# Performance work log

Hardware: AMD Instinct MI355X
Metric: run time of the kernel (lower is better)

The kernel has to match this reference:

```python
import jax, jax.numpy as jnp
import numpy as np

N = 50000
E = 800000
TEXT_VOCAB = 7000
ACTION_DIM = 64
MAX_POS = 5120
POS_DIM = 128   # edge encoder out_dim
NODE_DIM = 128  # text_out 64 + type_out 64
EDGE_DIM = 128
H1 = 256
OUT = 32
NEG_SLOPE = 0.2


def _pos_table():
    # sinusoidal table, [MAX_POS+1, POS_DIM]; even cols = cos, odd cols = sin
    positions = np.arange(0, MAX_POS + 1, dtype=np.float32)
    inv_freq = 1.0 / (10000.0 ** (np.arange(0.0, POS_DIM, 2.0, dtype=np.float32) / POS_DIM))
    si = np.outer(positions, inv_freq)
    tab = np.zeros((MAX_POS + 1, POS_DIM), dtype=np.float32)
    tab[:, 1::2] = np.sin(si)
    tab[:, 0::2] = np.cos(si)
    return jnp.asarray(tab)


def setup_inputs() -> dict:
    key = jax.random.key(0)
    ks = jax.random.split(key, 32)
    ri = jax.random.randint
    nrm = lambda k, s, scale=0.05: (jax.random.normal(k, s, dtype=jnp.float32) * scale)
    x = jnp.stack([ri(ks[0], (N,), 0, TEXT_VOCAB + 1, dtype=jnp.int32),
                   ri(ks[1], (N,), 0, 3, dtype=jnp.int32)], axis=-1)
    edge_index = ri(ks[2], (2, E), 0, N, dtype=jnp.int32)
    edge_attr = jnp.stack([ri(ks[3], (E,), 0, 3, dtype=jnp.int32),
                           ri(ks[4], (E,), 0, MAX_POS + 1, dtype=jnp.int32)], axis=-1)
    d = {
        "x": x, "edge_index": edge_index, "edge_attr": edge_attr,
        "text_emb": nrm(ks[5], (TEXT_VOCAB + 1, 64), 1.0),
        "type_emb": nrm(ks[6], (3, 64), 1.0),
        "flow_emb": nrm(ks[7], (3, EDGE_DIM), 1.0),
        "pos_table": _pos_table(),
        "pos_W": nrm(ks[8], (POS_DIM, POS_DIM)), "pos_b": nrm(ks[9], (POS_DIM,)),
        "c1_Wl": nrm(ks[10], (NODE_DIM, H1)), "c1_bl": nrm(ks[11], (H1,)),
        "c1_Wr": nrm(ks[12], (NODE_DIM, H1)), "c1_br": nrm(ks[13], (H1,)),
        "c1_We": nrm(ks[14], (EDGE_DIM, H1)), "c1_att": nrm(ks[15], (H1,)),
        "c1_bias": nrm(ks[16], (H1,)),
        "c2_Wl": nrm(ks[17], (H1, OUT)), "c2_bl": nrm(ks[18], (OUT,)),
        "c2_Wr": nrm(ks[19], (H1, OUT)), "c2_br": nrm(ks[20], (OUT,)),
        "c2_We": nrm(ks[21], (EDGE_DIM, OUT)), "c2_att": nrm(ks[22], (OUT,)),
        "c2_bias": nrm(ks[23], (OUT,)),
        "policy_W": nrm(ks[24], (OUT, ACTION_DIM), 0.2), "policy_b": nrm(ks[25], (ACTION_DIM,)),
    }
    return d


def gatv2(h, src, dst, ea, Wl, bl, Wr, br, We, att, bias, n):
    # PyG GATv2Conv, heads=1, add_self_loops=True, fill_value='mean'
    loop_attr = jnp.broadcast_to(ea.mean(0), (n, ea.shape[1]))
    s = jnp.concatenate([src, jnp.arange(n, dtype=src.dtype)])
    d = jnp.concatenate([dst, jnp.arange(n, dtype=dst.dtype)])
    ea_full = jnp.concatenate([ea, loop_attr], axis=0)
    xl = h @ Wl + bl  # messages (source side)
    xr = h @ Wr + br  # destination side
    m = xl[s] + xr[d] + ea_full @ We          # [E+n, F]
    e = jnp.where(m > 0, m, NEG_SLOPE * m) @ att  # per-edge logit [E+n]
    emax = jax.ops.segment_max(e, d, num_segments=n)
    a = jnp.exp(e - emax[d])
    denom = jax.ops.segment_sum(a, d, num_segments=n)
    alpha = a / denom[d]
    return jax.ops.segment_sum(alpha[:, None] * xl[s], d, num_segments=n) + bias


def reference(x, edge_index, edge_attr, text_emb, type_emb, flow_emb, pos_table,
              pos_W, pos_b,
              c1_Wl, c1_bl, c1_Wr, c1_br, c1_We, c1_att, c1_bias,
              c2_Wl, c2_bl, c2_Wr, c2_br, c2_We, c2_att, c2_bias,
              policy_W, policy_b):
    # NodeEncoder: concat of text and type embeddings -> [N, 128]
    h = jnp.concatenate([text_emb[x[:, 0]], type_emb[x[:, 1]]], axis=-1)
    # EdgeEncoder: flow embedding + linear(position sinusoid embedding)
    pos = edge_attr[:, 1]
    pos = jnp.where(pos > MAX_POS, pos, MAX_POS)  # faithful to original .where usage
    pos = jnp.clip(pos, 0, MAX_POS)
    ea = flow_emb[edge_attr[:, 0]] + (pos_table[pos] @ pos_W + pos_b)  # [E, 128]
    src, dst = edge_index[0], edge_index[1]
    h = gatv2(h, src, dst, ea, c1_Wl, c1_bl, c1_Wr, c1_br, c1_We, c1_att, c1_bias, h.shape[0])
    h = gatv2(h, src, dst, ea, c2_Wl, c2_bl, c2_Wr, c2_br, c2_We, c2_att, c2_bias, h.shape[0])
    g = h.mean(0)  # [32] graph readout
    logits = g @ policy_W + policy_b
    return jax.nn.softmax(logits, axis=-1)
```

## Files before the change

### kernel.cpp

```cpp
#include <hip/hip_runtime.h>

#define NEG_SLOPE 0.2f

typedef __attribute__((ext_vector_type(8))) short bf16x8;
typedef __attribute__((ext_vector_type(4))) float f32x4;

static __device__ __forceinline__ float lrelu(float m) {
    return fmaf(0.4f, fabsf(m), 0.6f * m);
}

static __device__ __forceinline__ float wsum64(float v) {
#pragma unroll
    for (int off = 32; off >= 1; off >>= 1) v += __shfl_xor(v, off, 64);
    return v;
}
static __device__ __forceinline__ float wsum32(float v) {
#pragma unroll
    for (int off = 16; off >= 1; off >>= 1) v += __shfl_xor(v, off, 64);
    return v;
}
static __device__ __forceinline__ float wmax64(float v) {
#pragma unroll
    for (int off = 32; off >= 1; off >>= 1) v = fmaxf(v, __shfl_xor(v, off, 64));
    return v;
}

static __device__ __forceinline__ unsigned short bf16r(float a) {
    unsigned int u = __float_as_uint(a);
    return (unsigned short)((u + 0x7FFFu + ((u >> 16) & 1u)) >> 16);
}
static __device__ __forceinline__ unsigned int bf16pack(float a, float b) {
    unsigned int ua = __float_as_uint(a);
    ua = (ua + 0x7FFFu + ((ua >> 16) & 1u)) >> 16;
    unsigned int ub = __float_as_uint(b);
    ub = (ub + 0x7FFFu + ((ub >> 16) & 1u)) & 0xFFFF0000u;
    return ua | ub;
}
static __device__ __forceinline__ float bfld(unsigned short s) {
    return __uint_as_float((unsigned int)s << 16);
}
static __device__ __forceinline__ float4 bf16x4_to_f4(uint2 u) {
    float4 v;
    v.x = __uint_as_float(u.x << 16);
    v.y = __uint_as_float(u.x & 0xFFFF0000u);
    v.z = __uint_as_float(u.y << 16);
    v.w = __uint_as_float(u.y & 0xFFFF0000u);
    return v;
}

static __device__ __forceinline__ float ldot4(const float4 xs, const float4 pre,
                                              const float4 av) {
    float q;
    q  = lrelu(xs.x + pre.x) * av.x;
    q += lrelu(xs.y + pre.y) * av.y;
    q += lrelu(xs.z + pre.z) * av.z;
    q += lrelu(xs.w + pre.w) * av.w;
    return q;
}

__global__ void k_zero_all(int* __restrict__ cntw, int n, int* __restrict__ cnt3,
                           int* __restrict__ gsum) {
    int i = blockIdx.x * blockDim.x + threadIdx.x;
    if (i < n) cntw[i] = 0;
    if (i < 4) cnt3[i] = 0;
    if (i < 32) gsum[i] = 0;
}

__global__ void k_edges(const int* __restrict__ ei, const int* __restrict__ ea,
                        int* __restrict__ cnt, int* __restrict__ cnt3, int E) {
    __shared__ int sh3[3];
    if (threadIdx.x < 3) sh3[threadIdx.x] = 0;
    __syncthreads();
    int e = blockIdx.x * blockDim.x + threadIdx.x;
    if (e < E) {
        atomicAdd(&cnt[ei[E + e]], 1);
        int f = ea[2 * e];
        f = f < 0 ? 0 : (f > 2 ? 2 : f);
        atomicAdd(&sh3[f], 1);
    }
    __syncthreads();
    if (threadIdx.x < 3) atomicAdd(&cnt3[threadIdx.x], sh3[threadIdx.x]);
}

__global__ void k_prep(const float* __restrict__ pos_table, const float* __restrict__ pos_W,
                       const float* __restrict__ pos_b, const float* __restrict__ flow_emb,
                       const float* __restrict__ We1, const float* __restrict__ We2,
                       const int* __restrict__ cnt3,
                       float* __restrict__ eaW1, float* __restrict__ loopW1,
                       float* __restrict__ eaW2, float* __restrict__ loopW2, int E) {
    __shared__ float posc[128];
    __shared__ float lv[128];
    int t = threadIdx.x;
    if (t < 128) {
        const float* row = pos_table + 5120 * 128;
        float a = pos_b[t];
        for (int k = 0; k < 128; ++k) a += row[k] * pos_W[k * 128 + t];
        posc[t] = a;
        float invE = 1.0f / (float)E;
        lv[t] = ((float)cnt3[0] * flow_emb[t] + (float)cnt3[1] * flow_emb[128 + t] +
                 (float)cnt3[2] * flow_emb[256 + t]) * invE + a;
    }
    __syncthreads();
    {
        int j = t;
        float a0 = 0.f, a1 = 0.f, a2 = 0.f, al = 0.f;
        for (int k = 0; k < 128; ++k) {
            float w = We1[k * 256 + j];
            float pc = posc[k];
            a0 += (flow_emb[k] + pc) * w;
            a1 += (flow_emb[128 + k] + pc) * w;
            a2 += (flow_emb[256 + k] + pc) * w;
            al += lv[k] * w;
        }
        eaW1[j] = a0; eaW1[256 + j] = a1; eaW1[512 + j] = a2; loopW1[j] = al;
    }
    if (t < 32) {
        int j = t;
        float a0 = 0.f, a1 = 0.f, a2 = 0.f, al = 0.f;
        for (int k = 0; k < 128; ++k) {
            float w = We2[k * 32 + j];
            float pc = posc[k];
            a0 += (flow_emb[k] + pc) * w;
            a1 += (flow_emb[128 + k] + pc) * w;
            a2 += (flow_emb[256 + k] + pc) * w;
            al += lv[k] * w;
        }
        eaW2[j] = a0; eaW2[32 + j] = a1; eaW2[64 + j] = a2; loopW2[j] = al;
    }
}

__global__ void k_prepW(const float* __restrict__ Wl1, const float* __restrict__ Wr1,
                        const float* __restrict__ Wl2, const float* __restrict__ Wr2,
                        unsigned short* __restrict__ Bt1, unsigned short* __restrict__ Bt2) {
    int i = blockIdx.x * blockDim.x + threadIdx.x;
    if (i < 512 * 128) {
        int nn = i >> 7, k = i & 127;
        float v = (nn < 256) ? Wl1[(size_t)k * 256 + nn] : Wr1[(size_t)k * 256 + nn - 256];
        Bt1[i] = bf16r(v);
    } else {
        int j = i - 512 * 128;
        if (j < 64 * 256) {
            int nn = j >> 8, k = j & 255;
            float v = (nn < 32) ? Wl2[(size_t)k * 32 + nn] : Wr2[(size_t)k * 32 + nn - 32];
            Bt2[j] = bf16r(v);
        }
    }
}

__global__ __launch_bounds__(256) void k_scan_block(const int* __restrict__ cnt,
                                                    int* __restrict__ rowptr,
                                                    int* __restrict__ bsum, int n) {
    __shared__ int sh[256];
    int b = blockIdx.x, t = threadIdx.x;
    int base = b * 1024 + t * 4;
    int v0 = base + 0 < n ? cnt[base + 0] : 0;
    int v1 = base + 1 < n ? cnt[base + 1] : 0;
    int v2 = base + 2 < n ? cnt[base + 2] : 0;
    int v3 = base + 3 < n ? cnt[base + 3] : 0;
    int tot = v0 + v1 + v2 + v3;
    sh[t] = tot;
    __syncthreads();
    for (int off = 1; off < 256; off <<= 1) {
        int x = (t >= off) ? sh[t - off] : 0;
        __syncthreads();
        sh[t] += x;
        __syncthreads();
    }
    int excl = (t > 0) ? sh[t - 1] : 0;
    if (base + 0 < n) rowptr[base + 0] = excl;
    if (base + 1 < n) rowptr[base + 1] = excl + v0;
    if (base + 2 < n) rowptr[base + 2] = excl + v0 + v1;
    if (base + 3 < n) rowptr[base + 3] = excl + v0 + v1 + v2;
    if (t == 255) bsum[b] = sh[255];
}

__global__ void k_scan_top(int* __restrict__ bsum, int* __restrict__ rowptr, int nb, int n) {
    if (threadIdx.x == 0 && blockIdx.x == 0) {
        int run = 0;
        for (int b = 0; b < nb; ++b) { int x = bsum[b]; bsum[b] = run; run += x; }
        rowptr[n] = run;
    }
}

__global__ void k_scan_add(int* __restrict__ rowptr, const int* __restrict__ bsum,
                           int* __restrict__ wptr, int n) {
    int i = blockIdx.x * blockDim.x + threadIdx.x;
    if (i < n) {
        int v = rowptr[i] + bsum[i >> 10];
        rowptr[i] = v;
        wptr[i] = v;
    }
}

__global__ void k_scatter(const int* __restrict__ ei, const int* __restrict__ ea,
                          int* __restrict__ wptr, int* __restrict__ packed, int E) {
    int e = blockIdx.x * blockDim.x + threadIdx.x;
    if (e >= E) return;
    int s = ei[e], d = ei[E + e];
    int f = ea[2 * e];
    f = f < 0 ? 0 : (f > 2 ? 2 : f);
    int p = atomicAdd(&wptr[d], 1);
    packed[p] = (s & 0xFFFF) | (f << 16);
}

__global__ __launch_bounds__(256) void k_gemm1(const int* __restrict__ x,
        const float* __restrict__ text_emb, const float* __restrict__ type_emb,
        const unsigned short* __restrict__ Bt,
        const float* __restrict__ bl, const float* __restrict__ br,
        unsigned short* __restrict__ xc, int n) {
    __shared__ unsigned short Ash[64][136];
    __shared__ unsigned short Bsh[128][136];
    int t = threadIdx.x;
    int node0 = blockIdx.x * 64;
    for (int i = t; i < 64 * 128; i += 256) {
        int r = i >> 7, cc = i & 127;
        int nd = node0 + r;
        float v = 0.f;
        if (nd < n)
            v = (cc < 64) ? text_emb[(size_t)x[nd * 2] * 64 + cc]
                          : type_emb[(size_t)x[nd * 2 + 1] * 64 + (cc - 64)];
        Ash[r][cc] = bf16r(v);
    }
    int wave = t >> 6, lane = t & 63;
    int m = lane & 15, q = lane >> 4;
    for (int nb = 0; nb < 4; ++nb) {
        __syncthreads();
        for (int i = t; i < 128 * 16; i += 256) {
            int r = i >> 4, cs = i & 15;
            uint4 v = ((const uint4*)(Bt + (size_t)(nb * 128 + r) * 128))[cs];
            *(uint4*)&Bsh[r][cs * 8] = v;
        }
        __syncthreads();
        f32x4 acc[8];
#pragma unroll
        for (int nt = 0; nt < 8; ++nt) acc[nt] = (f32x4){0.f, 0.f, 0.f, 0.f};
#pragma unroll
        for (int k = 0; k < 128; k += 32) {
            bf16x8 a = *(const bf16x8*)&Ash[wave * 16 + m][k + q * 8];
#pragma unroll
            for (int nt = 0; nt < 8; ++nt) {
                bf16x8 b = *(const bf16x8*)&Bsh[nt * 16 + m][k + q * 8];
                acc[nt] = __builtin_amdgcn_mfma_f32_16x16x32_bf16(a, b, acc[nt], 0, 0, 0);
            }
        }
#pragma unroll
        for (int r = 0; r < 4; ++r) {
            int node = node0 + wave * 16 + q * 4 + r;
            if (node < n) {
                unsigned short* rowp = xc + (size_t)node * 512 + nb * 128 + m;
#pragma unroll
                for (int nt = 0; nt < 8; ++nt) {
                    int ng = nb * 128 + nt * 16 + m;
                    float bv = (ng < 256) ? bl[ng] : br[ng - 256];
                    rowp[nt * 16] = bf16r(acc[nt][r] + bv);
                }
            }
        }
    }
}

__global__ __launch_bounds__(256) void k_gemm2(const unsigned short* __restrict__ h2b,
        const unsigned short* __restrict__ Bt,
        const float* __restrict__ bl, const float* __restrict__ br,
        unsigned short* __restrict__ xc, int n) {
    __shared__ unsigned short Ash[32][264];
    __shared__ unsigned short Bsh[64][264];
    int t = threadIdx.x;
    int node0 = blockIdx.x * 32;
    for (int i = t; i < 32 * 32; i += 256) {
        int r = i >> 5, cs = i & 31;
        int nd = node0 + r;
        uint4 v = make_uint4(0u, 0u, 0u, 0u);
        if (nd < n) v = ((const uint4*)(h2b + (size_t)nd * 256))[cs];
        *(uint4*)&Ash[r][cs * 8] = v;
    }
    for (int i = t; i < 64 * 32; i += 256) {
        int r = i >> 5, cs = i & 31;
        uint4 v = ((const uint4*)(Bt + (size_t)r * 256))[cs];
        *(uint4*)&Bsh[r][cs * 8] = v;
    }
    __syncthreads();
    int wave = t >> 6, lane = t & 63;
    int m = lane & 15, q = lane >> 4;
    int mrow = (wave >> 1) * 16;
    int nh   = (wave & 1) * 32;
    f32x4 acc[2];
    acc[0] = (f32x4){0.f, 0.f, 0.f, 0.f};
    acc[1] = (f32x4){0.f, 0.f, 0.f, 0.f};
#pragma unroll
    for (int k = 0; k < 256; k += 32) {
        bf16x8 a = *(const bf16x8*)&Ash[mrow + m][k + q * 8];
#pragma unroll
        for (int nt = 0; nt < 2; ++nt) {
            bf16x8 b = *(const bf16x8*)&Bsh[nh + nt * 16 + m][k + q * 8];
            acc[nt] = __builtin_amdgcn_mfma_f32_16x16x32_bf16(a, b, acc[nt], 0, 0, 0);
        }
    }
#pragma unroll
    for (int r = 0; r < 4; ++r) {
        int node = node0 + mrow + q * 4 + r;
        if (node < n) {
#pragma unroll
            for (int nt = 0; nt < 2; ++nt) {
                int ng = nh + nt * 16 + m;
                float bv = (ng < 32) ? bl[ng] : br[ng - 32];
                xc[(size_t)node * 64 + ng] = bf16r(acc[nt][r] + bv);
            }
        }
    }
}

__global__ __launch_bounds__(256) void k_gat256(const unsigned short* __restrict__ xc1,
        const int* __restrict__ rowptr, const int* __restrict__ packed,
        const float* __restrict__ eaW, const float* __restrict__ loopW,
        const float* __restrict__ att, const float* __restrict__ bias,
        unsigned short* __restrict__ h2b, int n) {
    int wid = (blockIdx.x * blockDim.x + threadIdx.x) >> 6;
    int lane = threadIdx.x & 63;
    if (wid >= n) return;
    int d = wid;
    int c = lane * 4;
    float4 xld = bf16x4_to_f4(((const uint2*)(xc1 + (size_t)d * 512))[lane]);
    float4 xrd = bf16x4_to_f4(((const uint2*)(xc1 + (size_t)d * 512 + 256))[lane]);
    float4 av  = *(const float4*)(att + c);
    float4 r0 = *(const float4*)(eaW + c);
    float4 r1 = *(const float4*)(eaW + 256 + c);
    float4 r2 = *(const float4*)(eaW + 512 + c);
    r0.x += xrd.x; r0.y += xrd.y; r0.z += xrd.z; r0.w += xrd.w;
    r1.x += xrd.x; r1.y += xrd.y; r1.z += xrd.z; r1.w += xrd.w;
    r2.x += xrd.x; r2.y += xrd.y; r2.z += xrd.z; r2.w += xrd.w;
    float4 lw = *(const float4*)(loopW + c);
    float4 sl; sl.x = xrd.x + lw.x; sl.y = xrd.y + lw.y;
    sl.z = xrd.z + lw.z; sl.w = xrd.w + lw.w;
    float q = wsum64(ldot4(xld, sl, av));
    float wself = __expf(q);
    float den = wself;
    float4 acc;
    acc.x = wself * xld.x; acc.y = wself * xld.y;
    acc.z = wself * xld.z; acc.w = wself * xld.w;

    int p0 = rowptr[d], p1 = rowptr[d + 1];
    int p = p0;
    for (; p + 4 <= p1; p += 4) {
        int pk0 = packed[p], pk1 = packed[p + 1];
        int pk2 = packed[p + 2], pk3 = packed[p + 3];
        uint2 u0 = ((const uint2*)(xc1 + (size_t)(pk0 & 0xFFFF) * 512))[lane];
        uint2 u1 = ((const uint2*)(xc1 + (size_t)(pk1 & 0xFFFF) * 512))[lane];
        uint2 u2 = ((const uint2*)(xc1 + (size_t)(pk2 & 0xFFFF) * 512))[lane];
        uint2 u3 = ((const uint2*)(xc1 + (size_t)(pk3 & 0xFFFF) * 512))[lane];
        float4 xs0 = bf16x4_to_f4(u0);
        float4 xs1 = bf16x4_to_f4(u1);
        float4 xs2 = bf16x4_to_f4(u2);
        float4 xs3 = bf16x4_to_f4(u3);
        int f0 = pk0 >> 16, f1 = pk1 >> 16, f2 = pk2 >> 16, f3 = pk3 >> 16;
        float4 pr0 = (f0 == 0) ? r0 : ((f0 == 1) ? r1 : r2);
        float4 pr1 = (f1 == 0) ? r0 : ((f1 == 1) ? r1 : r2);
        float4 pr2 = (f2 == 0) ? r0 : ((f2 == 1) ? r1 : r2);
        float4 pr3 = (f3 == 0) ? r0 : ((f3 == 1) ? r1 : r2);
        float q0 = ldot4(xs0, pr0, av);
        float q1 = ldot4(xs1, pr1, av);
        float q2 = ldot4(xs2, pr2, av);
        float q3 = ldot4(xs3, pr3, av);
#pragma unroll
        for (int off = 32; off >= 1; off >>= 1) {
            q0 += __shfl_xor(q0, off, 64);
            q1 += __shfl_xor(q1, off, 64);
            q2 += __shfl_xor(q2, off, 64);
            q3 += __shfl_xor(q3, off, 64);
        }
        float w0 = __expf(q0), w1 = __expf(q1);
        float w2 = __expf(q2), w3 = __expf(q3);
        den += (w0 + w1) + (w2 + w3);
        acc.x += w0 * xs0.x + w1 * xs1.x + w2 * xs2.x + w3 * xs3.x;
        acc.y += w0 * xs0.y + w1 * xs1.y + w2 * xs2.y + w3 * xs3.y;
        acc.z += w0 * xs0.z + w1 * xs1.z + w2 * xs2.z + w3 * xs3.z;
        acc.w += w0 * xs0.w + w1 * xs1.w + w2 * xs2.w + w3 * xs3.w;
    }
    for (; p < p1; ++p) {
        int pk = packed[p];
        float4 xs = bf16x4_to_f4(((const uint2*)(xc1 + (size_t)(pk & 0xFFFF) * 512))[lane]);
        int f = pk >> 16;
        float4 pr = (f == 0) ? r0 : ((f == 1) ? r1 : r2);
        float qq = wsum64(ldot4(xs, pr, av));
        float w = __expf(qq);
        den += w;
        acc.x += w * xs.x; acc.y += w * xs.y; acc.z += w * xs.z; acc.w += w * xs.w;
    }
    float inv = 1.f / den;
    float4 bv = *(const float4*)(bias + c);
    float4 o;
    o.x = acc.x * inv + bv.x; o.y = acc.y * inv + bv.y;
    o.z = acc.z * inv + bv.z; o.w = acc.w * inv + bv.w;
    ((uint2*)(h2b + (size_t)d * 256))[lane] =
        make_uint2(bf16pack(o.x, o.y), bf16pack(o.z, o.w));
}

__global__ __launch_bounds__(256) void k_gat32(const unsigned short* __restrict__ xc2,
        const int* __restrict__ rowptr, const int* __restrict__ packed,
        const float* __restrict__ eaW, const float* __restrict__ loopW,
        const float* __restrict__ att, const float* __restrict__ bias,
        float* __restrict__ out, int n) {
    int wid = (blockIdx.x * blockDim.x + threadIdx.x) >> 6;
    int lane = threadIdx.x & 63;
    if (wid >= n) return;
    int d = wid;
    int half = lane >> 5;
    int c = lane & 31;
    float xld = bfld(xc2[(size_t)d * 64 + c]);
    float xrd = bfld(xc2[(size_t)d * 64 + 32 + c]);
    float av = att[c];
    float r0 = eaW[c] + xrd, r1 = eaW[32 + c] + xrd, r2 = eaW[64 + c] + xrd;
    float den = 0.f, acc = 0.f;
    if (half == 0) {
        float lw = loopW[c];
        float q = wsum32(lrelu(xld + xrd + lw) * av);
        float wself = __expf(q);
        den = wself;
        acc = wself * xld;
    }
    int p0 = rowptr[d], p1 = rowptr[d + 1];
    int p = p0 + half;
    for (; p + 2 < p1; p += 4) {
        int pkA = packed[p], pkB = packed[p + 2];
        float xsA = bfld(xc2[(size_t)(pkA & 0xFFFF) * 64 + c]);
        float xsB = bfld(xc2[(size_t)(pkB & 0xFFFF) * 64 + c]);
        int fA = pkA >> 16, fB = pkB >> 16;
        float prA = (fA == 0) ? r0 : ((fA == 1) ? r1 : r2);
        float prB = (fB == 0) ? r0 : ((fB == 1) ? r1 : r2);
        float qA = lrelu(xsA + prA) * av;
        float qB = lrelu(xsB + prB) * av;
#pragma unroll
        for (int off = 16; off >= 1; off >>= 1) {
            qA += __shfl_xor(qA, off, 64);
            qB += __shfl_xor(qB, off, 64);
        }
        float wA = __expf(qA), wB = __expf(qB);
        den += wA + wB;
        acc += wA * xsA + wB * xsB;
    }
    for (; p < p1; p += 2) {
        int pk = packed[p];
        float xs = bfld(xc2[(size_t)(pk & 0xFFFF) * 64 + c]);
        int f = pk >> 16;
        float pr = (f == 0) ? r0 : ((f == 1) ? r1 : r2);
        float q = wsum32(lrelu(xs + pr) * av);
        float w = __expf(q);
        den += w;
        acc += w * xs;
    }
    den += __shfl_xor(den, 32, 64);
    acc += __shfl_xor(acc, 32, 64);
    if (lane < 32) out[(size_t)d * 32 + c] = acc / den + bias[c];
}

__global__ __launch_bounds__(256) void k_mean(const float* __restrict__ out2,
                                              float* __restrict__ gsum, int n) {
    __shared__ float sh[256];
    int t = threadIdx.x;
    int c = t & 31, g = t >> 5;
    float acc = 0.f;
    for (int nd = blockIdx.x * 8 + g; nd < n; nd += gridDim.x * 8)
        acc += out2[(size_t)nd * 32 + c];
    sh[t] = acc;
    __syncthreads();
    if (t < 32) {
        float s2 = 0.f;
#pragma unroll
        for (int gg = 0; gg < 8; ++gg) s2 += sh[gg * 32 + c];
        atomicAdd(&gsum[c], s2);
    }
}

__global__ void k_final(const float* __restrict__ gsum, const float* __restrict__ policy_W,
                        const float* __restrict__ policy_b, float* __restrict__ out, int n) {
    int t = threadIdx.x;
    float invN = 1.0f / (float)n;
    float acc = policy_b[t];
    for (int cc = 0; cc < 32; ++cc) acc += gsum[cc] * invN * policy_W[cc * 64 + t];
    float mx = wmax64(acc);
    float ex = __expf(acc - mx);
    float s = wsum64(ex);
    out[t] = ex / s;
}

extern "C" void kernel_launch(void* const* d_in, const int* in_sizes, int n_in,
                              void* d_out, int out_size, void* d_ws, size_t ws_size,
                              hipStream_t stream) {
    const int* x          = (const int*)d_in[0];
    const int* edge_index = (const int*)d_in[1];
    const int* edge_attr  = (const int*)d_in[2];
    const float* text_emb = (const float*)d_in[3];
    const float* type_emb = (const float*)d_in[4];
    const float* flow_emb = (const float*)d_in[5];
    const float* pos_table= (const float*)d_in[6];
    const float* pos_W    = (const float*)d_in[7];
    const float* pos_b    = (const float*)d_in[8];
    const float* c1_Wl    = (const float*)d_in[9];
    const float* c1_bl    = (const float*)d_in[10];
    const float* c1_Wr    = (const float*)d_in[11];
    const float* c1_br    = (const float*)d_in[12];
    const float* c1_We    = (const float*)d_in[13];
    const float* c1_att   = (const float*)d_in[14];
    const float* c1_bias  = (const float*)d_in[15];
    const float* c2_Wl    = (const float*)d_in[16];
    const float* c2_bl    = (const float*)d_in[17];
    const float* c2_Wr    = (const float*)d_in[18];
    const float* c2_br    = (const float*)d_in[19];
    const float* c2_We    = (const float*)d_in[20];
    const float* c2_att   = (const float*)d_in[21];
    const float* c2_bias  = (const float*)d_in[22];
    const float* policy_W = (const float*)d_in[23];
    const float* policy_b = (const float*)d_in[24];
    float* out = (float*)d_out;

    const int N = in_sizes[0] / 2;
    const int E = in_sizes[1] / 2;

    char* base = (char*)d_ws;
    size_t off = 0;
    auto alloc = [&](size_t bytes) -> void* {
        void* p = base + off;
        off = (off + bytes + 255) & ~(size_t)255;
        return p;
    };
    unsigned short* xc1  = (unsigned short*)alloc((size_t)N * 512 * 2);
    unsigned short* h2b  = (unsigned short*)alloc((size_t)N * 256 * 2);
    unsigned short* xc2  = (unsigned short*)alloc((size_t)N * 64 * 2);
    float*          out2 = (float*)alloc((size_t)N * 32 * 4);
    unsigned short* Bt1  = (unsigned short*)alloc((size_t)512 * 128 * 2);
    unsigned short* Bt2  = (unsigned short*)alloc((size_t)64 * 256 * 2);
    int*            cntw   = (int*)alloc((size_t)N * 4);
    int*            rowptr = (int*)alloc((size_t)(N + 1) * 4);
    int*            packed = (int*)alloc((size_t)E * 4);
    int*            bsum   = (int*)alloc(64 * 4);
    int*            cnt3   = (int*)alloc(4 * 4);
    float*          eaW1   = (float*)alloc(768 * 4);
    float*          loopW1 = (float*)alloc(256 * 4);
    float*          eaW2   = (float*)alloc(96 * 4);
    float*          loopW2 = (float*)alloc(32 * 4);
    float*          gsum   = (float*)alloc(32 * 4);

    k_zero_all<<<(N + 255) / 256, 256, 0, stream>>>(cntw, N, cnt3, (int*)gsum);

    k_edges<<<(E + 255) / 256, 256, 0, stream>>>(edge_index, edge_attr, cntw, cnt3, E);
    k_prep<<<1, 256, 0, stream>>>(pos_table, pos_W, pos_b, flow_emb, c1_We, c2_We,
                                  cnt3, eaW1, loopW1, eaW2, loopW2, E);
    k_prepW<<<(512 * 128 + 64 * 256 + 255) / 256, 256, 0, stream>>>(
        c1_Wl, c1_Wr, c2_Wl, c2_Wr, Bt1, Bt2);

    int nb = (N + 1023) / 1024;
    k_scan_block<<<nb, 256, 0, stream>>>(cntw, rowptr, bsum, N);
    k_scan_top<<<1, 64, 0, stream>>>(bsum, rowptr, nb, N);
    k_scan_add<<<(N + 255) / 256, 256, 0, stream>>>(rowptr, bsum, cntw, N);
    k_scatter<<<(E + 255) / 256, 256, 0, stream>>>(edge_index, edge_attr, cntw, packed, E);

    k_gemm1<<<(N + 63) / 64, 256, 0, stream>>>(x, text_emb, type_emb, Bt1,
                                               c1_bl, c1_br, xc1, N);
    k_gat256<<<(N + 3) / 4, 256, 0, stream>>>(xc1, rowptr, packed, eaW1, loopW1,
                                              c1_att, c1_bias, h2b, N);

    k_gemm2<<<(N + 31) / 32, 256, 0, stream>>>(h2b, Bt2, c2_bl, c2_br, xc2, N);
    k_gat32<<<(N + 3) / 4, 256, 0, stream>>>(xc2, rowptr, packed, eaW2, loopW2,
                                             c2_att, c2_bias, out2, N);

    k_mean<<<256, 256, 0, stream>>>(out2, gsum, N);
    k_final<<<1, 64, 0, stream>>>(gsum, policy_W, policy_b, out, N);
}
```

Measured before the change: 447.0 us.

## Bucket CSR by destination and flow type; process multiple edges per wave in GAT

The CSR is now keyed by (destination, flow type), so each node's edges are grouped by their edge-feature class. This removes the per-edge flow decode and select, and packed entries store only the source index. Both GAT kernels split each wave into lane groups that each handle a different edge with wider per-lane vectors (16 channels, or 4 for layer 2). The group partial sums are combined with cross-group shuffles at the end. The weight-prep kernel is merged into the prep launch, at the cost of a three-times-larger count/scan array and more registers per lane.

After: 514.4 us. 15.1% more time.

```diff
diff --git a/kernel.cpp b/kernel.cpp
--- a/kernel.cpp
+++ b/kernel.cpp
@@ -12,11 +12,6 @@
 static __device__ __forceinline__ float wsum64(float v) {
 #pragma unroll
     for (int off = 32; off >= 1; off >>= 1) v += __shfl_xor(v, off, 64);
-    return v;
-}
-static __device__ __forceinline__ float wsum32(float v) {
-#pragma unroll
-    for (int off = 16; off >= 1; off >>= 1) v += __shfl_xor(v, off, 64);
     return v;
 }
 static __device__ __forceinline__ float wmax64(float v) {
@@ -36,58 +31,75 @@
     ub = (ub + 0x7FFFu + ((ub >> 16) & 1u)) & 0xFFFF0000u;
     return ua | ub;
 }
-static __device__ __forceinline__ float bfld(unsigned short s) {
-    return __uint_as_float((unsigned int)s << 16);
-}
-static __device__ __forceinline__ float4 bf16x4_to_f4(uint2 u) {
-    float4 v;
-    v.x = __uint_as_float(u.x << 16);
-    v.y = __uint_as_float(u.x & 0xFFFF0000u);
-    v.z = __uint_as_float(u.y << 16);
-    v.w = __uint_as_float(u.y & 0xFFFF0000u);
-    return v;
-}
-
-static __device__ __forceinline__ float ldot4(const float4 xs, const float4 pre,
-                                              const float4 av) {
-    float q;
-    q  = lrelu(xs.x + pre.x) * av.x;
-    q += lrelu(xs.y + pre.y) * av.y;
-    q += lrelu(xs.z + pre.z) * av.z;
-    q += lrelu(xs.w + pre.w) * av.w;
-    return q;
-}
-
-__global__ void k_zero_all(int* __restrict__ cntw, int n, int* __restrict__ cnt3,
+static __device__ __forceinline__ void expand8(uint4 u, float* o) {
+    o[0] = __uint_as_float(u.x << 16); o[1] = __uint_as_float(u.x & 0xFFFF0000u);
+    o[2] = __uint_as_float(u.y << 16); o[3] = __uint_as_float(u.y & 0xFFFF0000u);
+    o[4] = __uint_as_float(u.z << 16); o[5] = __uint_as_float(u.z & 0xFFFF0000u);
+    o[6] = __uint_as_float(u.w << 16); o[7] = __uint_as_float(u.w & 0xFFFF0000u);
+}
+static __device__ __forceinline__ void expand4(uint2 u, float* o) {
+    o[0] = __uint_as_float(u.x << 16); o[1] = __uint_as_float(u.x & 0xFFFF0000u);
+    o[2] = __uint_as_float(u.y << 16); o[3] = __uint_as_float(u.y & 0xFFFF0000u);
+}
+static __device__ __forceinline__ void load16(const float* p, float* o) {
+#pragma unroll
+    for (int j = 0; j < 4; ++j) {
+        float4 v = ((const float4*)p)[j];
+        o[j * 4 + 0] = v.x; o[j * 4 + 1] = v.y; o[j * 4 + 2] = v.z; o[j * 4 + 3] = v.w;
+    }
+}
+
+__global__ void k_zero_all(int* __restrict__ cntF, int n3, int* __restrict__ cnt3,
                            int* __restrict__ gsum) {
     int i = blockIdx.x * blockDim.x + threadIdx.x;
-    if (i < n) cntw[i] = 0;
+    if (i < n3) cntF[i] = 0;
     if (i < 4) cnt3[i] = 0;
     if (i < 32) gsum[i] = 0;
 }
 
 __global__ void k_edges(const int* __restrict__ ei, const int* __restrict__ ea,
-                        int* __restrict__ cnt, int* __restrict__ cnt3, int E) {
+                        int* __restrict__ cntF, int* __restrict__ cnt3, int E) {
     __shared__ int sh3[3];
     if (threadIdx.x < 3) sh3[threadIdx.x] = 0;
     __syncthreads();
     int e = blockIdx.x * blockDim.x + threadIdx.x;
     if (e < E) {
-        atomicAdd(&cnt[ei[E + e]], 1);
+        int dd = ei[E + e];
         int f = ea[2 * e];
         f = f < 0 ? 0 : (f > 2 ? 2 : f);
+        atomicAdd(&cntF[dd * 3 + f], 1);
         atomicAdd(&sh3[f], 1);
     }
     __syncthreads();
     if (threadIdx.x < 3) atomicAdd(&cnt3[threadIdx.x], sh3[threadIdx.x]);
 }
 
-__global__ void k_prep(const float* __restrict__ pos_table, const float* __restrict__ pos_W,
-                       const float* __restrict__ pos_b, const float* __restrict__ flow_emb,
-                       const float* __restrict__ We1, const float* __restrict__ We2,
-                       const int* __restrict__ cnt3,
-                       float* __restrict__ eaW1, float* __restrict__ loopW1,
-                       float* __restrict__ eaW2, float* __restrict__ loopW2, int E) {
+__global__ void k_prep_all(const float* __restrict__ pos_table, const float* __restrict__ pos_W,
+                           const float* __restrict__ pos_b, const float* __restrict__ flow_emb,
+                           const float* __restrict__ We1, const float* __restrict__ We2,
+                           const int* __restrict__ cnt3,
+                           float* __restrict__ eaW1, float* __restrict__ loopW1,
+                           float* __restrict__ eaW2, float* __restrict__ loopW2,
+                           const float* __restrict__ Wl1, const float* __restrict__ Wr1,
+                           const float* __restrict__ Wl2, const float* __restrict__ Wr2,
+                           unsigned short* __restrict__ Bt1, unsigned short* __restrict__ Bt2,
+                           int E) {
+    if (blockIdx.x != 0) {
+        int i = (blockIdx.x - 1) * 256 + threadIdx.x;
+        if (i < 512 * 128) {
+            int nn = i >> 7, k = i & 127;
+            float v = (nn < 256) ? Wl1[(size_t)k * 256 + nn] : Wr1[(size_t)k * 256 + nn - 256];
+            Bt1[i] = bf16r(v);
+        } else {
+            int j = i - 512 * 128;
+            if (j < 64 * 256) {
+                int nn = j >> 8, k = j & 255;
+                float v = (nn < 32) ? Wl2[(size_t)k * 32 + nn] : Wr2[(size_t)k * 32 + nn - 32];
+                Bt2[j] = bf16r(v);
+            }
+        }
+        return;
+    }
     __shared__ float posc[128];
     __shared__ float lv[128];
     int t = threadIdx.x;
@@ -126,24 +138,6 @@
             al += lv[k] * w;
         }
         eaW2[j] = a0; eaW2[32 + j] = a1; eaW2[64 + j] = a2; loopW2[j] = al;
-    }
-}
-
-__global__ void k_prepW(const float* __restrict__ Wl1, const float* __restrict__ Wr1,
-                        const float* __restrict__ Wl2, const float* __restrict__ Wr2,
-                        unsigned short* __restrict__ Bt1, unsigned short* __restrict__ Bt2) {
-    int i = blockIdx.x * blockDim.x + threadIdx.x;
-    if (i < 512 * 128) {
-        int nn = i >> 7, k = i & 127;
-        float v = (nn < 256) ? Wl1[(size_t)k * 256 + nn] : Wr1[(size_t)k * 256 + nn - 256];
-        Bt1[i] = bf16r(v);
-    } else {
-        int j = i - 512 * 128;
-        if (j < 64 * 256) {
-            int nn = j >> 8, k = j & 255;
-            float v = (nn < 32) ? Wl2[(size_t)k * 32 + nn] : Wr2[(size_t)k * 32 + nn - 32];
-            Bt2[j] = bf16r(v);
-        }
     }
 }
 
@@ -196,11 +190,11 @@
                           int* __restrict__ wptr, int* __restrict__ packed, int E) {
     int e = blockIdx.x * blockDim.x + threadIdx.x;
     if (e >= E) return;
-    int s = ei[e], d = ei[E + e];
+    int s = ei[e], dd = ei[E + e];
     int f = ea[2 * e];
     f = f < 0 ? 0 : (f > 2 ? 2 : f);
-    int p = atomicAdd(&wptr[d], 1);
-    packed[p] = (s & 0xFFFF) | (f << 16);
+    int p = atomicAdd(&wptr[dd * 3 + f], 1);
+    packed[p] = s;
 }
 
 __global__ __launch_bounds__(256) void k_gemm1(const int* __restrict__ x,
@@ -311,146 +305,225 @@
 }
 
 __global__ __launch_bounds__(256) void k_gat256(const unsigned short* __restrict__ xc1,
-        const int* __restrict__ rowptr, const int* __restrict__ packed,
+        const int* __restrict__ rowptrF, const int* __restrict__ packed,
         const float* __restrict__ eaW, const float* __restrict__ loopW,
         const float* __restrict__ att, const float* __restrict__ bias,
         unsigned short* __restrict__ h2b, int n) {
     int wid = (blockIdx.x * blockDim.x + threadIdx.x) >> 6;
+    if (wid >= n) return;
     int lane = threadIdx.x & 63;
-    if (wid >= n) return;
+    int g = lane >> 4, li = lane & 15;
     int d = wid;
-    int c = lane * 4;
-    float4 xld = bf16x4_to_f4(((const uint2*)(xc1 + (size_t)d * 512))[lane]);
-    float4 xrd = bf16x4_to_f4(((const uint2*)(xc1 + (size_t)d * 512 + 256))[lane]);
-    float4 av  = *(const float4*)(att + c);
-    float4 r0 = *(const float4*)(eaW + c);
-    float4 r1 = *(const float4*)(eaW + 256 + c);
-    float4 r2 = *(const float4*)(eaW + 512 + c);
-    r0.x += xrd.x; r0.y += xrd.y; r0.z += xrd.z; r0.w += xrd.w;
-    r1.x += xrd.x; r1.y += xrd.y; r1.z += xrd.z; r1.w += xrd.w;
-    r2.x += xrd.x; r2.y += xrd.y; r2.z += xrd.z; r2.w += xrd.w;
-    float4 lw = *(const float4*)(loopW + c);
-    float4 sl; sl.x = xrd.x + lw.x; sl.y = xrd.y + lw.y;
-    sl.z = xrd.z + lw.z; sl.w = xrd.w + lw.w;
-    float q = wsum64(ldot4(xld, sl, av));
-    float wself = __expf(q);
-    float den = wself;
-    float4 acc;
-    acc.x = wself * xld.x; acc.y = wself * xld.y;
-    acc.z = wself * xld.z; acc.w = wself * xld.w;
-
-    int p0 = rowptr[d], p1 = rowptr[d + 1];
-    int p = p0;
-    for (; p + 4 <= p1; p += 4) {
-        int pk0 = packed[p], pk1 = packed[p + 1];
-        int pk2 = packed[p + 2], pk3 = packed[p + 3];
-        uint2 u0 = ((const uint2*)(xc1 + (size_t)(pk0 & 0xFFFF) * 512))[lane];
-        uint2 u1 = ((const uint2*)(xc1 + (size_t)(pk1 & 0xFFFF) * 512))[lane];
-        uint2 u2 = ((const uint2*)(xc1 + (size_t)(pk2 & 0xFFFF) * 512))[lane];
-        uint2 u3 = ((const uint2*)(xc1 + (size_t)(pk3 & 0xFFFF) * 512))[lane];
-        float4 xs0 = bf16x4_to_f4(u0);
-        float4 xs1 = bf16x4_to_f4(u1);
-        float4 xs2 = bf16x4_to_f4(u2);
-        float4 xs3 = bf16x4_to_f4(u3);
-        int f0 = pk0 >> 16, f1 = pk1 >> 16, f2 = pk2 >> 16, f3 = pk3 >> 16;
-        float4 pr0 = (f0 == 0) ? r0 : ((f0 == 1) ? r1 : r2);
-        float4 pr1 = (f1 == 0) ? r0 : ((f1 == 1) ? r1 : r2);
-        float4 pr2 = (f2 == 0) ? r0 : ((f2 == 1) ? r1 : r2);
-        float4 pr3 = (f3 == 0) ? r0 : ((f3 == 1) ? r1 : r2);
-        float q0 = ldot4(xs0, pr0, av);
-        float q1 = ldot4(xs1, pr1, av);
-        float q2 = ldot4(xs2, pr2, av);
-        float q3 = ldot4(xs3, pr3, av);
-#pragma unroll
-        for (int off = 32; off >= 1; off >>= 1) {
-            q0 += __shfl_xor(q0, off, 64);
-            q1 += __shfl_xor(q1, off, 64);
-            q2 += __shfl_xor(q2, off, 64);
-            q3 += __shfl_xor(q3, off, 64);
-        }
-        float w0 = __expf(q0), w1 = __expf(q1);
-        float w2 = __expf(q2), w3 = __expf(q3);
-        den += (w0 + w1) + (w2 + w3);
-        acc.x += w0 * xs0.x + w1 * xs1.x + w2 * xs2.x + w3 * xs3.x;
-        acc.y += w0 * xs0.y + w1 * xs1.y + w2 * xs2.y + w3 * xs3.y;
-        acc.z += w0 * xs0.z + w1 * xs1.z + w2 * xs2.z + w3 * xs3.z;
-        acc.w += w0 * xs0.w + w1 * xs1.w + w2 * xs2.w + w3 * xs3.w;
-    }
-    for (; p < p1; ++p) {
-        int pk = packed[p];
-        float4 xs = bf16x4_to_f4(((const uint2*)(xc1 + (size_t)(pk & 0xFFFF) * 512))[lane]);
-        int f = pk >> 16;
-        float4 pr = (f == 0) ? r0 : ((f == 1) ? r1 : r2);
-        float qq = wsum64(ldot4(xs, pr, av));
-        float w = __expf(qq);
+    int cb = li * 16;
+    const uint4* rxl = (const uint4*)(xc1 + (size_t)d * 512);
+    const uint4* rxr = (const uint4*)(xc1 + (size_t)d * 512 + 256);
+    uint4 ul0 = rxl[li * 2], ul1 = rxl[li * 2 + 1];
+    uint4 ur0 = rxr[li * 2], ur1 = rxr[li * 2 + 1];
+    float xld[16], xrd[16];
+    expand8(ul0, xld); expand8(ul1, xld + 8);
+    expand8(ur0, xrd); expand8(ur1, xrd + 8);
+    float av[16], r0[16], r1[16], r2[16], lw[16];
+    load16(att + cb, av);
+    load16(eaW + cb, r0);
+    load16(eaW + 256 + cb, r1);
+    load16(eaW + 512 + cb, r2);
+    load16(loopW + cb, lw);
+#pragma unroll
+    for (int i = 0; i < 16; ++i) {
+        r0[i] += xrd[i]; r1[i] += xrd[i]; r2[i] += xrd[i]; lw[i] += xrd[i];
+    }
+    float qs = 0.f;
+#pragma unroll
+    for (int i = 0; i < 16; ++i) qs += lrelu(xld[i] + lw[i]) * av[i];
+    qs += __shfl_xor(qs, 1, 64); qs += __shfl_xor(qs, 2, 64);
+    qs += __shfl_xor(qs, 4, 64); qs += __shfl_xor(qs, 8, 64);
+    float wself = __expf(qs);
+    float den = (g == 0) ? wself : 0.f;
+    float acc[16];
+#pragma unroll
+    for (int i = 0; i < 16; ++i) acc[i] = (g == 0) ? wself * xld[i] : 0.f;
+
+    int b0 = rowptrF[d * 3], b1 = rowptrF[d * 3 + 1];
+    int b2 = rowptrF[d * 3 + 2], b3 = rowptrF[d * 3 + 3];
+
+    auto edge = [&](int p, const float* pre) {
+        int s = packed[p];
+        const uint4* rs = (const uint4*)(xc1 + (size_t)s * 512);
+        uint4 u0 = rs[li * 2], u1 = rs[li * 2 + 1];
+        float xs[16];
+        expand8(u0, xs); expand8(u1, xs + 8);
+        float qp = 0.f;
+#pragma unroll
+        for (int i = 0; i < 16; ++i) qp += lrelu(xs[i] + pre[i]) * av[i];
+        qp += __shfl_xor(qp, 1, 64); qp += __shfl_xor(qp, 2, 64);
+        qp += __shfl_xor(qp, 4, 64); qp += __shfl_xor(qp, 8, 64);
+        float w = __expf(qp);
         den += w;
-        acc.x += w * xs.x; acc.y += w * xs.y; acc.z += w * xs.z; acc.w += w * xs.w;
-    }
-    float inv = 1.f / den;
-    float4 bv = *(const float4*)(bias + c);
-    float4 o;
-    o.x = acc.x * inv + bv.x; o.y = acc.y * inv + bv.y;
-    o.z = acc.z * inv + bv.z; o.w = acc.w * inv + bv.w;
-    ((uint2*)(h2b + (size_t)d * 256))[lane] =
-        make_uint2(bf16pack(o.x, o.y), bf16pack(o.z, o.w));
+#pragma unroll
+        for (int i = 0; i < 16; ++i) acc[i] = fmaf(w, xs[i], acc[i]);
+    };
+    auto run = [&](int pA, int pB, const float* pre) {
+        int p = pA + g;
+        for (; p + 4 < pB; p += 8) {
+            int s0 = packed[p], s1 = packed[p + 4];
+            const uint4* ra = (const uint4*)(xc1 + (size_t)s0 * 512);
+            const uint4* rb = (const uint4*)(xc1 + (size_t)s1 * 512);
+            uint4 a0 = ra[li * 2], a1 = ra[li * 2 + 1];
+            uint4 c0 = rb[li * 2], c1 = rb[li * 2 + 1];
+            float xa[16], xb[16];
+            expand8(a0, xa); expand8(a1, xa + 8);
+            expand8(c0, xb); expand8(c1, xb + 8);
+            float qa = 0.f, qb = 0.f;
+#pragma unroll
+            for (int i = 0; i < 16; ++i) {
+                qa += lrelu(xa[i] + pre[i]) * av[i];
+                qb += lrelu(xb[i] + pre[i]) * av[i];
+            }
+#pragma unroll
+            for (int off = 1; off <= 8; off <<= 1) {
+                qa += __shfl_xor(qa, off, 64);
+                qb += __shfl_xor(qb, off, 64);
+            }
+            float wa = __expf(qa), wb = __expf(qb);
+            den += wa + wb;
+#pragma unroll
+            for (int i = 0; i < 16; ++i)
+                acc[i] = fmaf(wb, xb[i], fmaf(wa, xa[i], acc[i]));
+        }
+        if (p < pB) edge(p, pre);
+    };
+    run(b0, b1, r0);
+    run(b1, b2, r1);
+    run(b2, b3, r2);
+
+#pragma unroll
+    for (int i = 0; i < 16; ++i) {
+        acc[i] += __shfl_xor(acc[i], 16, 64);
+        acc[i] += __shfl_xor(acc[i], 32, 64);
+    }
+    den += __shfl_xor(den, 16, 64);
+    den += __shfl_xor(den, 32, 64);
+    if (g == 0) {
+        float bv[16];
+        load16(bias + cb, bv);
+        float inv = 1.f / den;
+        uint4 o0, o1;
+        o0.x = bf16pack(fmaf(acc[0], inv, bv[0]),  fmaf(acc[1], inv, bv[1]));
+        o0.y = bf16pack(fmaf(acc[2], inv, bv[2]),  fmaf(acc[3], inv, bv[3]));
+        o0.z = bf16pack(fmaf(acc[4], inv, bv[4]),  fmaf(acc[5], inv, bv[5]));
+        o0.w = bf16pack(fmaf(acc[6], inv, bv[6]),  fmaf(acc[7], inv, bv[7]));
+        o1.x = bf16pack(fmaf(acc[8], inv, bv[8]),  fmaf(acc[9], inv, bv[9]));
+        o1.y = bf16pack(fmaf(acc[10], inv, bv[10]), fmaf(acc[11], inv, bv[11]));
+        o1.z = bf16pack(fmaf(acc[12], inv, bv[12]), fmaf(acc[13], inv, bv[13]));
+        o1.w = bf16pack(fmaf(acc[14], inv, bv[14]), fmaf(acc[15], inv, bv[15]));
+        uint4* orow = (uint4*)(h2b + (size_t)d * 256);
+        orow[li * 2] = o0;
+        orow[li * 2 + 1] = o1;
+    }
 }
 
 __global__ __launch_bounds__(256) void k_gat32(const unsigned short* __restrict__ xc2,
-        const int* __restrict__ rowptr, const int* __restrict__ packed,
+        const int* __restrict__ rowptrF, const int* __restrict__ packed,
         const float* __restrict__ eaW, const float* __restrict__ loopW,
         const float* __restrict__ att, const float* __restrict__ bias,
         float* __restrict__ out, int n) {
     int wid = (blockIdx.x * blockDim.x + threadIdx.x) >> 6;
+    if (wid >= n) return;
     int lane = threadIdx.x & 63;
-    if (wid >= n) return;
+    int g = lane >> 3, li = lane & 7;
     int d = wid;
-    int half = lane >> 5;
-    int c = lane & 31;
-    float xld = bfld(xc2[(size_t)d * 64 + c]);
-    float xrd = bfld(xc2[(size_t)d * 64 + 32 + c]);
-    float av = att[c];
-    float r0 = eaW[c] + xrd, r1 = eaW[32 + c] + xrd, r2 = eaW[64 + c] + xrd;
-    float den = 0.f, acc = 0.f;
-    if (half == 0) {
-        float lw = loopW[c];
-        float q = wsum32(lrelu(xld + xrd + lw) * av);
-        float wself = __expf(q);
-        den = wself;
-        acc = wself * xld;
-    }
-    int p0 = rowptr[d], p1 = rowptr[d + 1];
-    int p = p0 + half;
-    for (; p + 2 < p1; p += 4) {
-        int pkA = packed[p], pkB = packed[p + 2];
-        float xsA = bfld(xc2[(size_t)(pkA & 0xFFFF) * 64 + c]);
-        float xsB = bfld(xc2[(size_t)(pkB & 0xFFFF) * 64 + c]);
-        int fA = pkA >> 16, fB = pkB >> 16;
-        float prA = (fA == 0) ? r0 : ((fA == 1) ? r1 : r2);
-        float prB = (fB == 0) ? r0 : ((fB == 1) ? r1 : r2);
-        float qA = lrelu(xsA + prA) * av;
-        float qB = lrelu(xsB + prB) * av;
-#pragma unroll
-        for (int off = 16; off >= 1; off >>= 1) {
-            qA += __shfl_xor(qA, off, 64);
-            qB += __shfl_xor(qB, off, 64);
-        }
-        float wA = __expf(qA), wB = __expf(qB);
-        den += wA + wB;
-        acc += wA * xsA + wB * xsB;
-    }
-    for (; p < p1; p += 2) {
-        int pk = packed[p];
-        float xs = bfld(xc2[(size_t)(pk & 0xFFFF) * 64 + c]);
-        int f = pk >> 16;
-        float pr = (f == 0) ? r0 : ((f == 1) ? r1 : r2);
-        float q = wsum32(lrelu(xs + pr) * av);
-        float w = __expf(q);
+    int cb = li * 4;
+    uint2 uxl = ((const uint2*)(xc2 + (size_t)d * 64))[li];
+    uint2 uxr = ((const uint2*)(xc2 + (size_t)d * 64 + 32))[li];
+    float xld[4], xrd[4];
+    expand4(uxl, xld); expand4(uxr, xrd);
+    float4 avv = ((const float4*)att)[li];
+    float av[4] = {avv.x, avv.y, avv.z, avv.w};
+    float4 e0 = ((const float4*)eaW)[li];
+    float4 e1 = ((const float4*)(eaW + 32))[li];
+    float4 e2 = ((const float4*)(eaW + 64))[li];
+    float4 lwv = ((const float4*)loopW)[li];
+    float r0[4] = {e0.x + xrd[0], e0.y + xrd[1], e0.z + xrd[2], e0.w + xrd[3]};
+    float r1[4] = {e1.x + xrd[0], e1.y + xrd[1], e1.z + xrd[2], e1.w + xrd[3]};
+    float r2[4] = {e2.x + xrd[0], e2.y + xrd[1], e2.z + xrd[2], e2.w + xrd[3]};
+    float lw[4] = {lwv.x + xrd[0], lwv.y + xrd[1], lwv.z + xrd[2], lwv.w + xrd[3]};
+    float qs = 0.f;
+#pragma unroll
+    for (int i = 0; i < 4; ++i) qs += lrelu(xld[i] + lw[i]) * av[i];
+    qs += __shfl_xor(qs, 1, 64); qs += __shfl_xor(qs, 2, 64); qs += __shfl_xor(qs, 4, 64);
+    float wself = __expf(qs);
+    float den = (g == 0) ? wself : 0.f;
+    float acc[4];
+#pragma unroll
+    for (int i = 0; i < 4; ++i) acc[i] = (g == 0) ? wself * xld[i] : 0.f;
+
+    int b0 = rowptrF[d * 3], b1 = rowptrF[d * 3 + 1];
+    int b2 = rowptrF[d * 3 + 2], b3 = rowptrF[d * 3 + 3];
+
+    auto edge = [&](int p, const float* pre) {
+        int s = packed[p];
+        uint2 u = ((const uint2*)(xc2 + (size_t)s * 64))[li];
+        float xs[4];
+        expand4(u, xs);
+        float qp = 0.f;
+#pragma unroll
+        for (int i = 0; i < 4; ++i) qp += lrelu(xs[i] + pre[i]) * av[i];
+        qp += __shfl_xor(qp, 1, 64); qp += __shfl_xor(qp, 2, 64); qp += __shfl_xor(qp, 4, 64);
+        float w = __expf(qp);
         den += w;
-        acc += w * xs;
-    }
+#pragma unroll
+        for (int i = 0; i < 4; ++i) acc[i] = fmaf(w, xs[i], acc[i]);
+    };
+    auto run = [&](int pA, int pB, const float* pre) {
+        int p = pA + g;
+        for (; p + 8 < pB; p += 16) {
+            int s0 = packed[p], s1 = packed[p + 8];
+            uint2 ua = ((const uint2*)(xc2 + (size_t)s0 * 64))[li];
+            uint2 ub = ((const uint2*)(xc2 + (size_t)s1 * 64))[li];
+            float xa[4], xb[4];
+            expand4(ua, xa); expand4(ub, xb);
+            float qa = 0.f, qb = 0.f;
+#pragma unroll
+            for (int i = 0; i < 4; ++i) {
+                qa += lrelu(xa[i] + pre[i]) * av[i];
+                qb += lrelu(xb[i] + pre[i]) * av[i];
+            }
+#pragma unroll
+            for (int off = 1; off <= 4; off <<= 1) {
+                qa += __shfl_xor(qa, off, 64);
+                qb += __shfl_xor(qb, off, 64);
+            }
+            float wa = __expf(qa), wb = __expf(qb);
+            den += wa + wb;
+#pragma unroll
+            for (int i = 0; i < 4; ++i)
+                acc[i] = fmaf(wb, xb[i], fmaf(wa, xa[i], acc[i]));
+        }
+        if (p < pB) edge(p, pre);
+    };
+    run(b0, b1, r0);
+    run(b1, b2, r1);
+    run(b2, b3, r2);
+
+#pragma unroll
+    for (int i = 0; i < 4; ++i) {
+        acc[i] += __shfl_xor(acc[i], 8, 64);
+        acc[i] += __shfl_xor(acc[i], 16, 64);
+        acc[i] += __shfl_xor(acc[i], 32, 64);
+    }
+    den += __shfl_xor(den, 8, 64);
+    den += __shfl_xor(den, 16, 64);
     den += __shfl_xor(den, 32, 64);
-    acc += __shfl_xor(acc, 32, 64);
-    if (lane < 32) out[(size_t)d * 32 + c] = acc / den + bias[c];
+    if (g == 0) {
+        float4 bvv = ((const float4*)bias)[li];
+        float inv = 1.f / den;
+        float4 o;
+        o.x = fmaf(acc[0], inv, bvv.x);
+        o.y = fmaf(acc[1], inv, bvv.y);
+        o.z = fmaf(acc[2], inv, bvv.z);
+        o.w = fmaf(acc[3], inv, bvv.w);
+        ((float4*)(out + (size_t)d * 32))[li] = o;
+    }
 }
 
 __global__ __launch_bounds__(256) void k_mean(const float* __restrict__ out2,
@@ -515,6 +588,7 @@
 
     const int N = in_sizes[0] / 2;
     const int E = in_sizes[1] / 2;
+    const int n3 = 3 * N;
 
     char* base = (char*)d_ws;
     size_t off = 0;
@@ -529,10 +603,10 @@
     float*          out2 = (float*)alloc((size_t)N * 32 * 4);
     unsigned short* Bt1  = (unsigned short*)alloc((size_t)512 * 128 * 2);
     unsigned short* Bt2  = (unsigned short*)alloc((size_t)64 * 256 * 2);
-    int*            cntw   = (int*)alloc((size_t)N * 4);
-    int*            rowptr = (int*)alloc((size_t)(N + 1) * 4);
+    int*            cntF   = (int*)alloc((size_t)n3 * 4);
+    int*            rowptrF= (int*)alloc((size_t)(n3 + 1) * 4);
     int*            packed = (int*)alloc((size_t)E * 4);
-    int*            bsum   = (int*)alloc(64 * 4);
+    int*            bsum   = (int*)alloc(256 * 4);
     int*            cnt3   = (int*)alloc(4 * 4);
     float*          eaW1   = (float*)alloc(768 * 4);
     float*          loopW1 = (float*)alloc(256 * 4);
@@ -540,27 +614,26 @@
     float*          loopW2 = (float*)alloc(32 * 4);
     float*          gsum   = (float*)alloc(32 * 4);
 
-    k_zero_all<<<(N + 255) / 256, 256, 0, stream>>>(cntw, N, cnt3, (int*)gsum);
-
-    k_edges<<<(E + 255) / 256, 256, 0, stream>>>(edge_index, edge_attr, cntw, cnt3, E);
-    k_prep<<<1, 256, 0, stream>>>(pos_table, pos_W, pos_b, flow_emb, c1_We, c2_We,
-                                  cnt3, eaW1, loopW1, eaW2, loopW2, E);
-    k_prepW<<<(512 * 128 + 64 * 256 + 255) / 256, 256, 0, stream>>>(
-        c1_Wl, c1_Wr, c2_Wl, c2_Wr, Bt1, Bt2);
-
-    int nb = (N + 1023) / 1024;
-    k_scan_block<<<nb, 256, 0, stream>>>(cntw, rowptr, bsum, N);
-    k_scan_top<<<1, 64, 0, stream>>>(bsum, rowptr, nb, N);
-    k_scan_add<<<(N + 255) / 256, 256, 0, stream>>>(rowptr, bsum, cntw, N);
-    k_scatter<<<(E + 255) / 256, 256, 0, stream>>>(edge_index, edge_attr, cntw, packed, E);
+    k_zero_all<<<(n3 + 255) / 256, 256, 0, stream>>>(cntF, n3, cnt3, (int*)gsum);
+
+    k_edges<<<(E + 255) / 256, 256, 0, stream>>>(edge_index, edge_attr, cntF, cnt3, E);
+    k_prep_all<<<1 + (512 * 128 + 64 * 256) / 256, 256, 0, stream>>>(
+        pos_table, pos_W, pos_b, flow_emb, c1_We, c2_We, cnt3,
+        eaW1, loopW1, eaW2, loopW2, c1_Wl, c1_Wr, c2_Wl, c2_Wr, Bt1, Bt2, E);
+
+    int nb = (n3 + 1023) / 1024;
+    k_scan_block<<<nb, 256, 0, stream>>>(cntF, rowptrF, bsum, n3);
+    k_scan_top<<<1, 64, 0, stream>>>(bsum, rowptrF, nb, n3);
+    k_scan_add<<<(n3 + 255) / 256, 256, 0, stream>>>(rowptrF, bsum, cntF, n3);
+    k_scatter<<<(E + 255) / 256, 256, 0, stream>>>(edge_index, edge_attr, cntF, packed, E);
 
     k_gemm1<<<(N + 63) / 64, 256, 0, stream>>>(x, text_emb, type_emb, Bt1,
                                                c1_bl, c1_br, xc1, N);
-    k_gat256<<<(N + 3) / 4, 256, 0, stream>>>(xc1, rowptr, packed, eaW1, loopW1,
+    k_gat256<<<(N + 3) / 4, 256, 0, stream>>>(xc1, rowptrF, packed, eaW1, loopW1,
                                               c1_att, c1_bias, h2b, N);
 
     k_gemm2<<<(N + 31) / 32, 256, 0, stream>>>(h2b, Bt2, c2_bl, c2_br, xc2, N);
-    k_gat32<<<(N + 3) / 4, 256, 0, stream>>>(xc2, rowptr, packed, eaW2, loopW2,
+    k_gat32<<<(N + 3) / 4, 256, 0, stream>>>(xc2, rowptrF, packed, eaW2, loopW2,
                                              c2_att, c2_bias, out2, N);
 
     k_mean<<<256, 256, 0, stream>>>(out2, gsum, N);
```
